# Kernel optimization log

Measured on AMD Instinct MI355X. Metric: run time of the kernel, lower is better.

The kernel has to match this reference:

```python
import jax, jax.numpy as jnp
import numpy as np
from jax import lax

B, L, R = 128, 256, 36
D_TXT, D_IMG, D_SOC = 768, 2048, 10
EPS = 0.05 ** 2        # geomloss blur=0.05, p=2 -> epsilon = blur^p
N_ITERS = 20           # fixed log-domain Sinkhorn iterations
GAMMA = 0.01


def _pcost(x, y):
    # x: [B,n,d], y: [B,m,d] -> C_ij = ||x_i - y_j||^2 / 2 (geomloss p=2 cost)
    xx = jnp.sum(x * x, -1)[:, :, None]
    yy = jnp.sum(y * y, -1)[:, None, :]
    xy = jnp.einsum('bnd,bmd->bnm', x, y)
    return 0.5 * (xx + yy - 2.0 * xy)


def _sinkhorn_cost(C, loga, logb, eps, n_iters):
    # Log-domain Sinkhorn; masked points carry loga/logb = -inf (zero weight).
    f = jnp.zeros(loga.shape, C.dtype)
    g = jnp.zeros(logb.shape, C.dtype)

    def body(fg, _):
        f, g = fg
        g = -eps * jax.nn.logsumexp(loga[:, :, None] + (f[:, :, None] - C) / eps, axis=1)
        f = -eps * jax.nn.logsumexp(logb[:, None, :] + (g[:, None, :] - C) / eps, axis=2)
        return (f, g), None

    (f, g), _ = lax.scan(body, (f, g), None, length=n_iters)
    a = jnp.exp(loga)  # exp(-inf) = 0 for masked entries
    b = jnp.exp(logb)
    return jnp.sum(a * f, -1) + jnp.sum(b * g, -1)  # <a,f> + <b,g>


def _forward(txt_global, txt_region, img_global, img_region, social, attn_mask,
             W_stat, b_stat, W_gt, b_gt, W_gi, b_gi, W_rt, b_rt, W_ri, b_ri,
             W_m1, b_m1, W_m2, b_m2):
    relu = jax.nn.relu
    soc = relu(social @ W_stat + b_stat)                            # [B,100]
    tg = relu(jnp.concatenate([txt_global, soc], axis=1) @ W_gt + b_gt)  # [B,200]
    ig = relu(img_global @ W_gi + b_gi)                              # [B,200]
    h = relu((tg + ig) @ W_m1 + b_m1)
    mix_pred = h @ W_m2 + b_m2                                       # [B,2]

    tr = relu(txt_region @ W_rt + b_rt)                              # [B,L,50]
    ir = relu(img_region @ W_ri + b_ri)                              # [B,R,50]

    Bn, _, _ = tr.shape
    Rn = ir.shape[1]
    mask = attn_mask > 0
    n_words = jnp.sum(attn_mask, axis=-1).astype(tr.dtype)          # [B]
    loga = jnp.where(mask, -jnp.log(n_words)[:, None], -jnp.inf)    # uniform over valid tokens
    logb = jnp.full((Bn, Rn), -jnp.log(float(Rn)), tr.dtype)        # uniform over regions

    # Debiased Sinkhorn divergence (geomloss SamplesLoss default debias=True):
    Sxy = _sinkhorn_cost(_pcost(tr, ir), loga, logb, EPS, N_ITERS)
    Sxx = _sinkhorn_cost(_pcost(tr, tr), loga, loga, EPS, N_ITERS)
    Syy = _sinkhorn_cost(_pcost(ir, ir), logb, logb, EPS, N_ITERS)
    w_dis = Sxy - 0.5 * (Sxx + Syy)                                  # [B]

    w_pred = jnp.stack([1.0 - GAMMA * w_dis, GAMMA * w_dis], axis=1)  # [B,2]
    logit = jax.nn.softmax(jnp.maximum(mix_pred, w_pred), axis=1)
    return logit


def setup_inputs() -> dict:
    key = jax.random.key(0)
    ks = jax.random.split(key, 24)
    init = lambda k, s: (jax.random.normal(k, s) * 0.02).astype(jnp.float32)
    lengths = jax.random.randint(ks[0], (B,), 16, L + 1)             # ragged lengths
    attn_mask = (jnp.arange(L)[None, :] < lengths[:, None]).astype(jnp.int32)
    return {
        'txt_global': jax.random.normal(ks[1], (B, D_TXT), jnp.float32),
        'txt_region': jax.random.normal(ks[2], (B, L, D_TXT), jnp.float32),
        'img_global': jax.random.normal(ks[3], (B, D_IMG), jnp.float32),
        'img_region': jax.random.normal(ks[4], (B, R, D_IMG), jnp.float32),
        'social': jax.random.normal(ks[5], (B, D_SOC), jnp.float32),
        'attn_mask': attn_mask,
        'W_stat': init(ks[6], (D_SOC, 100)), 'b_stat': jnp.zeros((100,), jnp.float32),
        'W_gt': init(ks[7], (868, 200)), 'b_gt': jnp.zeros((200,), jnp.float32),
        'W_gi': init(ks[8], (D_IMG, 200)), 'b_gi': jnp.zeros((200,), jnp.float32),
        'W_rt': init(ks[9], (D_TXT, 50)), 'b_rt': jnp.zeros((50,), jnp.float32),
        'W_ri': init(ks[10], (D_IMG, 50)), 'b_ri': jnp.zeros((50,), jnp.float32),
        'W_m1': init(ks[11], (200, 100)), 'b_m1': jnp.zeros((100,), jnp.float32),
        'W_m2': init(ks[12], (100, 2)), 'b_m2': jnp.zeros((2,), jnp.float32),
    }


def reference(txt_global, txt_region, img_global, img_region, social, attn_mask,
              W_stat, b_stat, W_gt, b_gt, W_gi, b_gi, W_rt, b_rt, W_ri, b_ri,
              W_m1, b_m1, W_m2, b_m2):
    return _forward(txt_global, txt_region, img_global, img_region, social, attn_mask,
                    W_stat, b_stat, W_gt, b_gt, W_gi, b_gi, W_rt, b_rt, W_ri, b_ri,
                    W_m1, b_m1, W_m2, b_m2)
```

## Files before the change

kernel.cpp:

```cpp
#include <hip/hip_runtime.h>

typedef float  f32x4 __attribute__((ext_vector_type(4)));
typedef short  s16x8 __attribute__((ext_vector_type(8)));

#define EPS_LN2      0.0017328679513998632f
#define INV_EPS_LN2  577.0780163555852f
#define LOG2_36      5.169925001442312f

__device__ __forceinline__ short f2bf(float x) {
  unsigned int u; __builtin_memcpy(&u, &x, 4);
  u = (u + 0x7FFFu + ((u >> 16) & 1u)) >> 16;
  return (short)u;
}

__global__ __launch_bounds__(256) void k_prep(
    const float* __restrict__ W_rt, const float* __restrict__ W_ri,
    short* __restrict__ frt, short* __restrict__ fri,
    const float* __restrict__ txt, const float* __restrict__ img,
    const float* __restrict__ social,
    const float* __restrict__ W_stat, const float* __restrict__ b_stat,
    const float* __restrict__ W_gt, const float* __restrict__ W_gi,
    float* __restrict__ pre) {
  __shared__ float sA[32][128];
  int bid = blockIdx.x;
  if (bid < 88) {
    int slot = bid * 256 + threadIdx.x;
    const float* W; short* dst; int f;
    if (slot < 6144) { W = W_rt; dst = frt; f = slot; }
    else             { W = W_ri; dst = fri; f = slot - 6144; }
    int k32 = f >> 8, rem = f & 255, ct = rem >> 6, l = rem & 63;
    int col = ct * 16 + (l & 15);
    int k0  = k32 * 32 + (l >> 4) * 8;
    s16x8 p;
#pragma unroll
    for (int c = 0; c < 8; ++c) {
      float v = (col < 50) ? W[(k0 + c) * 50 + col] : 0.f;
      p[c] = f2bf(v);
    }
    *(s16x8*)(dst + (long)f * 8) = p;
    return;
  }
  int gb = bid - 88;
  int job = gb >> 4, rb = (gb >> 2) & 3, cb = gb & 3;
  int t = threadIdx.x, r0 = rb * 32;
  const float* W; int k0, klen;
  if (job < 6)       { k0 = job * 128;       klen = 128; W = W_gt; }
  else if (job == 6) { k0 = 0;               klen = 100; W = W_gt + 768 * 200; }
  else               { k0 = (job - 7) * 128; klen = 128; W = W_gi; }
  if (job == 6) {
    for (int idx = t; idx < 4096; idx += 256) {
      int r = idx >> 7, k = idx & 127;
      float v = 0.f;
      if (k < 100) {
        v = b_stat[k];
#pragma unroll
        for (int u = 0; u < 10; ++u) v += social[(r0 + r) * 10 + u] * W_stat[u * 100 + k];
        v = fmaxf(v, 0.f);
      }
      sA[r][k] = v;
    }
  } else {
    const float* A = (job < 6) ? txt : img;
    int K_A = (job < 6) ? 768 : 2048;
    for (int idx = t; idx < 4096; idx += 256) {
      int r = idx >> 7, k = idx & 127;
      sA[r][k] = A[(r0 + r) * K_A + k0 + k];
    }
  }
  __syncthreads();
  int c = cb * 64 + (t & 63), rg = t >> 6;
  if (c < 200) {
    float acc[8];
#pragma unroll
    for (int i = 0; i < 8; ++i) acc[i] = 0.f;
    for (int k4 = 0; k4 < klen; k4 += 4) {
      float w0 = W[(k0 + k4    ) * 200 + c];
      float w1 = W[(k0 + k4 + 1) * 200 + c];
      float w2 = W[(k0 + k4 + 2) * 200 + c];
      float w3 = W[(k0 + k4 + 3) * 200 + c];
#pragma unroll
      for (int i = 0; i < 8; ++i) {
        f32x4 a = *(const f32x4*)&sA[rg * 8 + i][k4];
        acc[i] += a[0]*w0 + a[1]*w1 + a[2]*w2 + a[3]*w3;
      }
    }
    float* dst = pre + (long)job * 25600;
#pragma unroll
    for (int i = 0; i < 8; ++i)
      dst[(r0 + rg * 8 + i) * 200 + c] = acc[i];
  }
}

template<int K32>
__device__ __forceinline__ void proj_body(const float* __restrict__ A,
                                          const short* __restrict__ Bf,
                                          const float* __restrict__ bias,
                                          float* __restrict__ out, int bid,
                                          char* smem) {
  short* sB = (short*)smem;
  const int NWIN = K32 / 8;
  int wave = threadIdx.x >> 6, lane = threadIdx.x & 63;
  int rl = lane & 15, q = lane >> 4;
  int row0 = bid * 64 + wave * 16;
  const int K = K32 * 32;
  const float* ar = A + (long)(row0 + rl) * K + q * 8;
  int soff = wave * 4096 + lane * 8;

  f32x4 stage[8];
#pragma unroll
  for (int c = 0; c < 8; ++c)
    stage[c] = *(const f32x4*)(Bf + (long)soff + c * 512);
#pragma unroll
  for (int c = 0; c < 8; ++c)
    *(f32x4*)(sB + soff + c * 512) = stage[c];
  f32x4 a0 = *(const f32x4*)(ar);
  f32x4 a1 = *(const f32x4*)(ar + 4);
  f32x4 acc[4];
#pragma unroll
  for (int ct = 0; ct < 4; ++ct) acc[ct] = (f32x4){0.f, 0.f, 0.f, 0.f};
  __syncthreads();

  for (int w = 0; w < NWIN; ++w) {
    if (w + 1 < NWIN) {
      const short* src = Bf + (long)(w + 1) * 16384 + soff;
#pragma unroll
      for (int c = 0; c < 8; ++c) stage[c] = *(const f32x4*)(src + c * 512);
    }
    const short* bbuf = sB + (w & 1) * 16384;
#pragma unroll
    for (int kk8 = 0; kk8 < 8; ++kk8) {
      int k32 = w * 8 + kk8;
      f32x4 na0, na1;
      if (k32 + 1 < K32) {
        na0 = *(const f32x4*)(ar + (k32 + 1) * 32);
        na1 = *(const f32x4*)(ar + (k32 + 1) * 32 + 4);
      }
      s16x8 af;
      af[0]=f2bf(a0[0]); af[1]=f2bf(a0[1]); af[2]=f2bf(a0[2]); af[3]=f2bf(a0[3]);
      af[4]=f2bf(a1[0]); af[5]=f2bf(a1[1]); af[6]=f2bf(a1[2]); af[7]=f2bf(a1[3]);
      const short* bp = bbuf + kk8 * 2048 + lane * 8;
#pragma unroll
      for (int ct = 0; ct < 4; ++ct) {
        s16x8 bfr = *(const s16x8*)(bp + ct * 512);
        acc[ct] = __builtin_amdgcn_mfma_f32_16x16x32_bf16(af, bfr, acc[ct], 0, 0, 0);
      }
      a0 = na0; a1 = na1;
    }
    if (w + 1 < NWIN) {
      __syncthreads();
      short* nbuf = sB + ((w + 1) & 1) * 16384;
#pragma unroll
      for (int c = 0; c < 8; ++c) *(f32x4*)(nbuf + soff + c * 512) = stage[c];
      __syncthreads();
    }
  }
#pragma unroll
  for (int ct = 0; ct < 4; ++ct) {
    int col = ct * 16 + rl;
    float bv = (col < 50) ? bias[col] : 0.f;
#pragma unroll
    for (int r = 0; r < 4; ++r) {
      int grow = row0 + q * 4 + r;
      float o = fmaxf(acc[ct][r] + bv, 0.f);
      out[(long)grow * 64 + col] = (col < 50) ? o : 0.f;
    }
  }
}

__device__ __forceinline__ void mix_body(
    int r, const float* __restrict__ pre,
    const float* __restrict__ b_gt, const float* __restrict__ b_gi,
    const float* __restrict__ W_m1, const float* __restrict__ b_m1,
    const float* __restrict__ W_m2, const float* __restrict__ b_m2,
    float* __restrict__ mix, char* smem) {
  float* sm = (float*)smem;
  float* sh = (float*)(smem + 800);
  int t = threadIdx.x;
  if (t < 200) {
    float s1 = b_gt[t], s2 = b_gi[t];
#pragma unroll
    for (int j = 0; j < 7; ++j)  s1 += pre[(long)j * 25600 + r * 200 + t];
#pragma unroll
    for (int j = 7; j < 23; ++j) s2 += pre[(long)j * 25600 + r * 200 + t];
    sm[t] = fmaxf(s1, 0.f) + fmaxf(s2, 0.f);
  }
  __syncthreads();
  if (t < 100) {
    float a = b_m1[t];
#pragma unroll 4
    for (int k = 0; k < 200; ++k) a += sm[k] * W_m1[k * 100 + t];
    sh[t] = fmaxf(a, 0.f);
  }
  __syncthreads();
  if (t < 2) {
    float a = b_m2[t];
    for (int k = 0; k < 100; ++k) a += sh[k] * W_m2[k * 2 + t];
    mix[r * 2 + t] = a;
  }
}

__global__ __launch_bounds__(256)
__attribute__((amdgpu_waves_per_eu(4, 4)))
void k_pm(
    const float* __restrict__ txt_region, const short* __restrict__ frt,
    const float* __restrict__ b_rt, float* __restrict__ tr,
    const float* __restrict__ img_region, const short* __restrict__ fri,
    const float* __restrict__ b_ri, float* __restrict__ ir,
    const float* __restrict__ pre,
    const float* __restrict__ b_gt, const float* __restrict__ b_gi,
    const float* __restrict__ W_m1, const float* __restrict__ b_m1,
    const float* __restrict__ W_m2, const float* __restrict__ b_m2,
    float* __restrict__ mix) {
  __shared__ __align__(16) char smem[65536];
  int bid = blockIdx.x;
  if (bid < 128)      mix_body(bid, pre, b_gt, b_gi, W_m1, b_m1, W_m2, b_m2, mix, smem);
  else if (bid < 640) proj_body<24>(txt_region, frt, b_rt, tr, bid - 128, smem);
  else                proj_body<64>(img_region, fri, b_ri, ir, bid - 640, smem);
}

#define SK_SMEM 50736

__global__ __launch_bounds__(1024)
__attribute__((amdgpu_waves_per_eu(4, 4)))
void k_sink(
    const float* __restrict__ tr, const float* __restrict__ ir,
    const int* __restrict__ amask, float* __restrict__ Cxx,
    float* __restrict__ Sxy, float* __restrict__ Sxx, float* __restrict__ Syy) {
  __shared__ __align__(16) char smem[SK_SMEM];
  int role = blockIdx.x >> 7;
  int b    = blockIdx.x & 127;
  int tid  = threadIdx.x;

  if (role == 0) {
    short* Xf    = (short*)smem;
    float* norms = (float*)(smem + 32768);
    float* sA    = (float*)(smem + 33792);
    float* sF    = (float*)(smem + 34816);
    float* sG    = (float*)(smem + 35840);
    float* sPm   = (float*)(smem + 36864);
    int*   nsh   = (int*)  (smem + 40960);
    if (tid < 64) {
      int c = 0;
      for (int i = tid; i < 256; i += 64) c += amask[b * 256 + i];
#pragma unroll
      for (int o = 1; o < 64; o <<= 1) c += __shfl_xor(c, o);
      if (tid == 0) *nsh = c;
    }
    const float* Xg = tr + (long)b * 256 * 64;
    for (int slot = tid; slot < 2048; slot += 1024) {
      int t = slot >> 7, k32 = (slot >> 6) & 1, l = slot & 63;
      int row = t * 16 + (l & 15), k0 = k32 * 32 + (l >> 4) * 8;
      const float* src = Xg + row * 64 + k0;
      f32x4 a0 = *(const f32x4*)src, a1 = *(const f32x4*)(src + 4);
      s16x8 p;
      p[0]=f2bf(a0[0]); p[1]=f2bf(a0[1]); p[2]=f2bf(a0[2]); p[3]=f2bf(a0[3]);
      p[4]=f2bf(a1[0]); p[5]=f2bf(a1[1]); p[6]=f2bf(a1[2]); p[7]=f2bf(a1[3]);
      *(s16x8*)(Xf + slot * 8) = p;
    }
    __syncthreads();
    int n = *nsh;
    int wv = tid >> 6, lane = tid & 63, q = lane >> 4;
    f32x4 acc[16];
#pragma unroll
    for (int ct = 0; ct < 16; ++ct) acc[ct] = (f32x4){0.f, 0.f, 0.f, 0.f};
    s16x8 afr0 = *(const s16x8*)(Xf + ((wv * 2 + 0) * 64 + lane) * 8);
    s16x8 afr1 = *(const s16x8*)(Xf + ((wv * 2 + 1) * 64 + lane) * 8);
#pragma unroll
    for (int ct = 0; ct < 16; ++ct) {
      s16x8 b0 = *(const s16x8*)(Xf + ((ct * 2 + 0) * 64 + lane) * 8);
      s16x8 b1 = *(const s16x8*)(Xf + ((ct * 2 + 1) * 64 + lane) * 8);
      acc[ct] = __builtin_amdgcn_mfma_f32_16x16x32_bf16(afr0, b0, acc[ct], 0, 0, 0);
      acc[ct] = __builtin_amdgcn_mfma_f32_16x16x32_bf16(afr1, b1, acc[ct], 0, 0, 0);
    }
#pragma unroll
    for (int r = 0; r < 4; ++r) {
      int m_ = q * 4 + r;
      if ((lane & 15) == m_) norms[wv * 16 + m_] = acc[wv][r];
    }
    __syncthreads();
    float* Cwb = Cxx + (long)b * 65536;
    if (wv * 16 < n) {
#pragma unroll
      for (int ct = 0; ct < 16; ++ct) {
        int gj = ct * 16 + (lane & 15);
        float nj = norms[gj];
#pragma unroll
        for (int r = 0; r < 4; ++r) {
          int gi = wv * 16 + q * 4 + r;
          Cwb[gi * 256 + gj] = (acc[ct][r] - 0.5f * (norms[gi] + nj)) * INV_EPS_LN2;
        }
      }
    }
    __syncthreads();
    int kk = tid >> 8, j = tid & 255, i0 = kk * 64;
    int iend = n - i0; if (iend > 64) iend = 64;
    float Creg[64];
    if (j < n) {
#pragma unroll
      for (int ch = 0; ch < 4; ++ch) {
        if (ch * 16 < iend) {
#pragma unroll
          for (int u = 0; u < 16; ++u)
            Creg[ch * 16 + u] = Cwb[(i0 + ch * 16 + u) * 256 + j];
        }
      }
    }
    float log2n = log2f((float)n);
    if (tid < 256) { sF[tid] = 0.f; sA[tid] = (tid < n) ? -log2n : -1e30f; }
    __syncthreads();
    const float* ap = sA + i0;
    for (int h = 0; h < 40; ++h) {
      float m = -1e30f;
      if (j < n) {
#pragma unroll
        for (int ch = 0; ch < 4; ++ch) {
          if (ch * 16 < iend) {
            const float* app = ap + ch * 16;
            f32x4 A0 = *(const f32x4*)(app);
            f32x4 A1 = *(const f32x4*)(app + 4);
            f32x4 A2 = *(const f32x4*)(app + 8);
            f32x4 A3 = *(const f32x4*)(app + 12);
            float x0 = A0[0]+Creg[ch*16+0],  x1 = A0[1]+Creg[ch*16+1];
            float x2 = A0[2]+Creg[ch*16+2],  x3 = A0[3]+Creg[ch*16+3];
            float x4 = A1[0]+Creg[ch*16+4],  x5 = A1[1]+Creg[ch*16+5];
            float x6 = A1[2]+Creg[ch*16+6],  x7 = A1[3]+Creg[ch*16+7];
            float x8 = A2[0]+Creg[ch*16+8],  x9 = A2[1]+Creg[ch*16+9];
            float xa = A2[2]+Creg[ch*16+10], xb = A2[3]+Creg[ch*16+11];
            float xc = A3[0]+Creg[ch*16+12], xd = A3[1]+Creg[ch*16+13];
            float xe = A3[2]+Creg[ch*16+14], xf = A3[3]+Creg[ch*16+15];
            float y0 = fmaxf(fmaxf(x0, x1), x2);
            float y1 = fmaxf(fmaxf(x3, x4), x5);
            float y2 = fmaxf(fmaxf(x6, x7), x8);
            float y3 = fmaxf(fmaxf(x9, xa), xb);
            float y4 = fmaxf(fmaxf(xc, xd), xe);
            float z0 = fmaxf(fmaxf(y0, y1), y2);
            float z1 = fmaxf(fmaxf(y3, y4), xf);
            m = fmaxf(fmaxf(m, z0), z1);
          }
        }
      }
      sPm[kk * 256 + j] = m;
      __syncthreads();
      if (tid < 256) {
        float m4 = fmaxf(fmaxf(sPm[tid], sPm[256 + tid]),
                         fmaxf(sPm[512 + tid], sPm[768 + tid]));
        if (tid < n) {
          ((h & 1) ? sF : sG)[tid] = -EPS_LN2 * m4;
          sA[tid] = -log2n - m4;
        }
      }
      __syncthreads();
    }
    if (tid < 64) {
      float a = 0.f;
      for (int i = tid; i < n; i += 64) a += sF[i] + sG[i];
#pragma unroll
      for (int o = 1; o < 64; o <<= 1) a += __shfl_xor(a, o);
      if (tid == 0) Sxx[b] = a / n;
    }
  } else if (role == 1) {
    float* Ys  = (float*)smem;
    float* Cs  = (float*)(smem + 9216);
    float* nx  = (float*)(smem + 47104);
    float* ny  = (float*)(smem + 48128);
    float* sA  = (float*)(smem + 48288);
    float* sB  = (float*)(smem + 49376);
    float* sF  = (float*)(smem + 49536);
    float* sG  = (float*)(smem + 50560);
    int*   nsh = (int*)  (smem + 50720);
    if (tid < 64) {
      int c = 0;
      for (int i = tid; i < 256; i += 64) c += amask[b * 256 + i];
#pragma unroll
      for (int o = 1; o < 64; o <<= 1) c += __shfl_xor(c, o);
      if (tid == 0) *nsh = c;
    }
    const float* Xg = tr + (long)b * 256 * 64;
    const float* Yg = ir + (long)b * 36 * 64;
    for (int idx = tid; idx < 576; idx += 1024) {
      int row = idx >> 4, q4 = idx & 15;
      *(f32x4*)(Ys + row * 64 + q4 * 4) = *(const f32x4*)(Yg + row * 64 + q4 * 4);
    }
    __syncthreads();
    int n = *nsh;
    if (tid < 256) {
      float a = 0.f;
#pragma unroll
      for (int q4 = 0; q4 < 13; ++q4) {
        f32x4 v = *(const f32x4*)(Xg + tid * 64 + q4 * 4);
        a += v[0]*v[0] + v[1]*v[1] + v[2]*v[2] + v[3]*v[3];
      }
      nx[tid] = a;
    } else if (tid < 292) {
      int jj = tid - 256; float a = 0.f;
#pragma unroll
      for (int q4 = 0; q4 < 13; ++q4) {
        f32x4 v = *(const f32x4*)(Ys + jj * 64 + q4 * 4);
        a += v[0]*v[0] + v[1]*v[1] + v[2]*v[2] + v[3]*v[3];
      }
      ny[jj] = a;
    }
    __syncthreads();
    if (tid < 1008) {
      int ii = tid / 36, jj = tid - ii * 36;
      f32x4 yr[13];
#pragma unroll
      for (int q4 = 0; q4 < 13; ++q4) yr[q4] = *(const f32x4*)(Ys + jj * 64 + q4 * 4);
      float nyj = ny[jj];
      for (int i = ii; i < 256; i += 28) {
        float d = 0.f;
#pragma unroll
        for (int q4 = 0; q4 < 13; ++q4) {
          f32x4 xv = *(const f32x4*)(Xg + i * 64 + q4 * 4);
          d += xv[0]*yr[q4][0] + xv[1]*yr[q4][1] + xv[2]*yr[q4][2] + xv[3]*yr[q4][3];
        }
        Cs[i * 37 + jj] = (d - 0.5f * (nx[i] + nyj)) * INV_EPS_LN2;
      }
    }
    __syncthreads();
    int jg = tid >> 4, kg = tid & 15;
    float Cg[16];
    if (jg < 36) {
#pragma unroll
      for (int t = 0; t < 16; ++t) Cg[t] = Cs[(kg * 16 + t) * 37 + jg];
    }
    int fi = tid >> 2, kf = tid & 3;
    float Cf[9];
#pragma unroll
    for (int t = 0; t < 9; ++t) {
      int jj2 = kf * 9 + t;
      Cf[t] = (jj2 < 36) ? Cs[fi * 37 + jj2] : 0.f;
    }
    float log2n = log2f((float)n);
    if (tid < 256) { sF[tid] = 0.f; sA[tid + (tid >> 4)] = -log2n; }
    __syncthreads();
    const float* agp = sA + kg * 17;
    int gend = n - kg * 16; if (gend > 16) gend = 16;
    for (int it = 0; it < 20; ++it) {
      float gm = -1e30f;
      if (jg < 36) {
#pragma unroll
        for (int t = 0; t < 16; ++t)
          if (t < gend) gm = fmaxf(gm, agp[t] + Cg[t]);
        gm = fmaxf(gm, __shfl_xor(gm, 1)); gm = fmaxf(gm, __shfl_xor(gm, 2));
        gm = fmaxf(gm, __shfl_xor(gm, 4)); gm = fmaxf(gm, __shfl_xor(gm, 8));
      }
      __syncthreads();
      if (jg < 36 && kg == 0) {
        sG[jg] = -EPS_LN2 * gm;
        sB[jg] = -LOG2_36 - gm;
      }
      __syncthreads();
      float fm = -1e30f;
#pragma unroll
      for (int t = 0; t < 9; ++t) {
        int jj2 = kf * 9 + t;
        if (jj2 < 36) fm = fmaxf(fm, sB[jj2] + Cf[t]);
      }
      fm = fmaxf(fm, __shfl_xor(fm, 1)); fm = fmaxf(fm, __shfl_xor(fm, 2));
      __syncthreads();
      if (kf == 0 && fi < n) {
        sF[fi] = -EPS_LN2 * fm;
        sA[fi + (fi >> 4)] = -log2n - fm;
      }
      __syncthreads();
    }
    if (tid < 64) {
      float a = 0.f;
      for (int i = tid; i < n; i += 64) a += sF[i];
      float g = (tid < 36) ? sG[tid] : 0.f;
#pragma unroll
      for (int o = 1; o < 64; o <<= 1) { a += __shfl_xor(a, o); g += __shfl_xor(g, o); }
      if (tid == 0) Sxy[b] = a / n + g / 36.f;
    }
  } else {
    float* Ys = (float*)smem;
    float* Cs = (float*)(smem + 9216);
    float* ny = (float*)(smem + 48128);
    float* sA = (float*)(smem + 48288);
    float* sF = (float*)(smem + 49536);
    float* sG = (float*)(smem + 50560);
    const float* Yg = ir + (long)b * 36 * 64;
    for (int idx = tid; idx < 576; idx += 1024) {
      int row = idx >> 4, q4 = idx & 15;
      *(f32x4*)(Ys + row * 64 + q4 * 4) = *(const f32x4*)(Yg + row * 64 + q4 * 4);
    }
    __syncthreads();
    if (tid < 36) {
      float a = 0.f;
#pragma unroll
      for (int q4 = 0; q4 < 13; ++q4) {
        f32x4 v = *(const f32x4*)(Ys + tid * 64 + q4 * 4);
        a += v[0]*v[0] + v[1]*v[1] + v[2]*v[2] + v[3]*v[3];
      }
      ny[tid] = a;
    }
    __syncthreads();
    if (tid < 1008) {
      int ii = tid / 36, jj = tid - ii * 36;
      f32x4 yr[13];
#pragma unroll
      for (int q4 = 0; q4 < 13; ++q4) yr[q4] = *(const f32x4*)(Ys + jj * 64 + q4 * 4);
      float nyj = ny[jj];
      for (int i = ii; i < 36; i += 28) {
        float d = 0.f;
#pragma unroll
        for (int q4 = 0; q4 < 13; ++q4) {
          f32x4 xv = *(const f32x4*)(Ys + i * 64 + q4 * 4);
          d += xv[0]*yr[q4][0] + xv[1]*yr[q4][1] + xv[2]*yr[q4][2] + xv[3]*yr[q4][3];
        }
        Cs[i * 37 + jj] = (d - 0.5f * (ny[i] + nyj)) * INV_EPS_LN2;
      }
    }
    __syncthreads();
    int j = tid >> 2, kk = tid & 3;
    float Creg[9];
    if (j < 36) {
#pragma unroll
      for (int t = 0; t < 9; ++t) {
        int i2 = kk * 9 + t;
        Creg[t] = (i2 < 36) ? Cs[i2 * 37 + j] : 0.f;
      }
    }
    if (tid < 36) { sF[tid] = 0.f; sA[tid] = -LOG2_36; }
    __syncthreads();
    for (int h = 0; h < 40; ++h) {
      float m = -1e30f;
      if (j < 36) {
#pragma unroll
        for (int t = 0; t < 9; ++t) {
          int i2 = kk * 9 + t;
          if (i2 < 36) m = fmaxf(m, sA[i2] + Creg[t]);
        }
        m = fmaxf(m, __shfl_xor(m, 1)); m = fmaxf(m, __shfl_xor(m, 2));
      }
      __syncthreads();
      if (j < 36 && kk == 0) {
        ((h & 1) ? sF : sG)[j] = -EPS_LN2 * m;
        sA[j] = -LOG2_36 - m;
      }
      __syncthreads();
    }
    if (tid < 64) {
      float a = (tid < 36) ? sF[tid] + sG[tid] : 0.f;
#pragma unroll
      for (int o = 1; o < 64; o <<= 1) a += __shfl_xor(a, o);
      if (tid == 0) Syy[b] = a / 36.f;
    }
  }
}

__global__ void k_final(const float* __restrict__ mix, const float* __restrict__ sxy,
                        const float* __restrict__ sxx, const float* __restrict__ syy,
                        float* __restrict__ out) {
  int b = blockIdx.x * 64 + threadIdx.x;
  if (b < 128) {
    float w  = sxy[b] - 0.5f * (sxx[b] + syy[b]);
    float x0 = fmaxf(mix[b * 2 + 0], 1.0f - 0.01f * w);
    float x1 = fmaxf(mix[b * 2 + 1], 0.01f * w);
    float mx = fmaxf(x0, x1);
    float e0 = expf(x0 - mx), e1 = expf(x1 - mx);
    float inv = 1.f / (e0 + e1);
    out[b * 2 + 0] = e0 * inv;
    out[b * 2 + 1] = e1 * inv;
  }
}

extern "C" void kernel_launch(void* const* d_in, const int* in_sizes, int n_in,
                              void* d_out, int out_size, void* d_ws, size_t ws_size,
                              hipStream_t stream) {
  const float* txt_global = (const float*)d_in[0];
  const float* txt_region = (const float*)d_in[1];
  const float* img_global = (const float*)d_in[2];
  const float* img_region = (const float*)d_in[3];
  const float* social     = (const float*)d_in[4];
  const int*   attn_mask  = (const int*)  d_in[5];
  const float* W_stat = (const float*)d_in[6];  const float* b_stat = (const float*)d_in[7];
  const float* W_gt   = (const float*)d_in[8];  const float* b_gt   = (const float*)d_in[9];
  const float* W_gi   = (const float*)d_in[10]; const float* b_gi   = (const float*)d_in[11];
  const float* W_rt   = (const float*)d_in[12]; const float* b_rt   = (const float*)d_in[13];
  const float* W_ri   = (const float*)d_in[14]; const float* b_ri   = (const float*)d_in[15];
  const float* W_m1   = (const float*)d_in[16]; const float* b_m1   = (const float*)d_in[17];
  const float* W_m2   = (const float*)d_in[18]; const float* b_m2   = (const float*)d_in[19];

  float* ws = (float*)d_ws;
  float* ws_mix = ws;
  float* ws_sxy = ws + 256;
  float* ws_sxx = ws + 384;
  float* ws_syy = ws + 512;
  short* ws_frt = (short*)(ws + 1024);
  short* ws_fri = (short*)(ws + 25600);
  float* ws_tr  = ws + 131072;
  float* ws_ir  = ws + 2228224;
  float* ws_cxx = ws + 2523136;
  float* ws_pre = ws_cxx;

  k_prep<<<456, 256, 0, stream>>>(W_rt, W_ri, ws_frt, ws_fri,
                                  txt_global, img_global, social,
                                  W_stat, b_stat, W_gt, W_gi, ws_pre);
  k_pm<<<712, 256, 0, stream>>>(txt_region, ws_frt, b_rt, ws_tr,
                                img_region, ws_fri, b_ri, ws_ir,
                                ws_pre, b_gt, b_gi,
                                W_m1, b_m1, W_m2, b_m2, ws_mix);
  k_sink<<<384, 1024, 0, stream>>>(ws_tr, ws_ir, attn_mask, ws_cxx,
                                   ws_sxy, ws_sxx, ws_syy);
  k_final<<<2, 64, 0, stream>>>(ws_mix, ws_sxy, ws_sxx, ws_syy, (float*)d_out);
}
```

Measured before the change: 342.4 us.

## Read projection weight fragments directly from global memory instead of LDS staging

The projection GEMM no longer stages the pre-packed bf16 weight windows through a 64KB double-buffered LDS buffer with barriers. Each wave now loads its B fragments straight from global memory, one k-step ahead, alongside the A rows. This removes the syncthreads and LDS traffic and cuts shared memory to a few hundred floats, and the waves-per-EU hint is relaxed to allow higher occupancy. In exchange every wave re-reads the same weights from global memory and relies on L2/L1 caching for that reuse.

```diff
diff --git a/kernel.cpp b/kernel.cpp
--- a/kernel.cpp
+++ b/kernel.cpp
@@ -95,64 +95,40 @@
 __device__ __forceinline__ void proj_body(const float* __restrict__ A,
                                           const short* __restrict__ Bf,
                                           const float* __restrict__ bias,
-                                          float* __restrict__ out, int bid,
-                                          char* smem) {
-  short* sB = (short*)smem;
-  const int NWIN = K32 / 8;
+                                          float* __restrict__ out, int bid) {
   int wave = threadIdx.x >> 6, lane = threadIdx.x & 63;
   int rl = lane & 15, q = lane >> 4;
   int row0 = bid * 64 + wave * 16;
   const int K = K32 * 32;
   const float* ar = A + (long)(row0 + rl) * K + q * 8;
-  int soff = wave * 4096 + lane * 8;
-
-  f32x4 stage[8];
-#pragma unroll
-  for (int c = 0; c < 8; ++c)
-    stage[c] = *(const f32x4*)(Bf + (long)soff + c * 512);
-#pragma unroll
-  for (int c = 0; c < 8; ++c)
-    *(f32x4*)(sB + soff + c * 512) = stage[c];
+  const s16x8* bp = (const s16x8*)Bf + lane;
+
+  f32x4 acc[4];
+#pragma unroll
+  for (int ct = 0; ct < 4; ++ct) acc[ct] = (f32x4){0.f, 0.f, 0.f, 0.f};
+
   f32x4 a0 = *(const f32x4*)(ar);
   f32x4 a1 = *(const f32x4*)(ar + 4);
-  f32x4 acc[4];
-#pragma unroll
-  for (int ct = 0; ct < 4; ++ct) acc[ct] = (f32x4){0.f, 0.f, 0.f, 0.f};
-  __syncthreads();
-
-  for (int w = 0; w < NWIN; ++w) {
-    if (w + 1 < NWIN) {
-      const short* src = Bf + (long)(w + 1) * 16384 + soff;
-#pragma unroll
-      for (int c = 0; c < 8; ++c) stage[c] = *(const f32x4*)(src + c * 512);
-    }
-    const short* bbuf = sB + (w & 1) * 16384;
-#pragma unroll
-    for (int kk8 = 0; kk8 < 8; ++kk8) {
-      int k32 = w * 8 + kk8;
-      f32x4 na0, na1;
-      if (k32 + 1 < K32) {
-        na0 = *(const f32x4*)(ar + (k32 + 1) * 32);
-        na1 = *(const f32x4*)(ar + (k32 + 1) * 32 + 4);
-      }
-      s16x8 af;
-      af[0]=f2bf(a0[0]); af[1]=f2bf(a0[1]); af[2]=f2bf(a0[2]); af[3]=f2bf(a0[3]);
-      af[4]=f2bf(a1[0]); af[5]=f2bf(a1[1]); af[6]=f2bf(a1[2]); af[7]=f2bf(a1[3]);
-      const short* bp = bbuf + kk8 * 2048 + lane * 8;
-#pragma unroll
-      for (int ct = 0; ct < 4; ++ct) {
-        s16x8 bfr = *(const s16x8*)(bp + ct * 512);
-        acc[ct] = __builtin_amdgcn_mfma_f32_16x16x32_bf16(af, bfr, acc[ct], 0, 0, 0);
-      }
-      a0 = na0; a1 = na1;
-    }
-    if (w + 1 < NWIN) {
-      __syncthreads();
-      short* nbuf = sB + ((w + 1) & 1) * 16384;
-#pragma unroll
-      for (int c = 0; c < 8; ++c) *(f32x4*)(nbuf + soff + c * 512) = stage[c];
-      __syncthreads();
-    }
+  s16x8 bf0 = bp[0], bf1 = bp[64], bf2 = bp[128], bf3 = bp[192];
+
+  for (int k32 = 0; k32 < K32; ++k32) {
+    f32x4 na0, na1;
+    s16x8 nb0, nb1, nb2, nb3;
+    if (k32 + 1 < K32) {
+      na0 = *(const f32x4*)(ar + (k32 + 1) * 32);
+      na1 = *(const f32x4*)(ar + (k32 + 1) * 32 + 4);
+      const s16x8* nbp = bp + (k32 + 1) * 256;
+      nb0 = nbp[0]; nb1 = nbp[64]; nb2 = nbp[128]; nb3 = nbp[192];
+    }
+    s16x8 af;
+    af[0]=f2bf(a0[0]); af[1]=f2bf(a0[1]); af[2]=f2bf(a0[2]); af[3]=f2bf(a0[3]);
+    af[4]=f2bf(a1[0]); af[5]=f2bf(a1[1]); af[6]=f2bf(a1[2]); af[7]=f2bf(a1[3]);
+    acc[0] = __builtin_amdgcn_mfma_f32_16x16x32_bf16(af, bf0, acc[0], 0, 0, 0);
+    acc[1] = __builtin_amdgcn_mfma_f32_16x16x32_bf16(af, bf1, acc[1], 0, 0, 0);
+    acc[2] = __builtin_amdgcn_mfma_f32_16x16x32_bf16(af, bf2, acc[2], 0, 0, 0);
+    acc[3] = __builtin_amdgcn_mfma_f32_16x16x32_bf16(af, bf3, acc[3], 0, 0, 0);
+    a0 = na0; a1 = na1;
+    bf0 = nb0; bf1 = nb1; bf2 = nb2; bf3 = nb3;
   }
 #pragma unroll
   for (int ct = 0; ct < 4; ++ct) {
@@ -172,9 +148,9 @@
     const float* __restrict__ b_gt, const float* __restrict__ b_gi,
     const float* __restrict__ W_m1, const float* __restrict__ b_m1,
     const float* __restrict__ W_m2, const float* __restrict__ b_m2,
-    float* __restrict__ mix, char* smem) {
-  float* sm = (float*)smem;
-  float* sh = (float*)(smem + 800);
+    float* __restrict__ mix, float* smem) {
+  float* sm = smem;
+  float* sh = smem + 200;
   int t = threadIdx.x;
   if (t < 200) {
     float s1 = b_gt[t], s2 = b_gi[t];
@@ -200,7 +176,7 @@
 }
 
 __global__ __launch_bounds__(256)
-__attribute__((amdgpu_waves_per_eu(4, 4)))
+__attribute__((amdgpu_waves_per_eu(4, 8)))
 void k_pm(
     const float* __restrict__ txt_region, const short* __restrict__ frt,
     const float* __restrict__ b_rt, float* __restrict__ tr,
@@ -211,11 +187,11 @@
     const float* __restrict__ W_m1, const float* __restrict__ b_m1,
     const float* __restrict__ W_m2, const float* __restrict__ b_m2,
     float* __restrict__ mix) {
-  __shared__ __align__(16) char smem[65536];
+  __shared__ __align__(16) float smem[304];
   int bid = blockIdx.x;
   if (bid < 128)      mix_body(bid, pre, b_gt, b_gi, W_m1, b_m1, W_m2, b_m2, mix, smem);
-  else if (bid < 640) proj_body<24>(txt_region, frt, b_rt, tr, bid - 128, smem);
-  else                proj_body<64>(img_region, fri, b_ri, ir, bid - 640, smem);
+  else if (bid < 640) proj_body<24>(txt_region, frt, b_rt, tr, bid - 128);
+  else                proj_body<64>(img_region, fri, b_ri, ir, bid - 640);
 }
 
 #define SK_SMEM 50736
```

Measured after the change: 336.3 us. Within noise of the previous version (-1.8%).
